# Performance work log

Hardware: AMD Instinct MI355X
Metric: run time of the kernel (lower is better)

## Reference

```python
import jax, jax.numpy as jnp
import numpy as np

D = 1024        # inputsize / d_model
G = 8           # groupnum (KV groups)
H = 16          # heads per group
DQ = 128        # qk head dim
DV = 128        # v head dim
FF = 1024       # ffoutsize
B, S = 1, 1024


def _rmsnorm(t, gamma, d_model):
    # torch F.normalize(x, dim=-1) * sqrt(d_model) * gamma
    n = jnp.sqrt(jnp.sum(t * t, axis=-1, keepdims=True))
    return t / jnp.maximum(n, 1e-12) * (d_model ** 0.5) * gamma


def setup_inputs() -> dict:
    key = jax.random.key(0)
    ks = jax.random.split(key, 8)
    std = 0.02
    x = jax.random.normal(ks[0], (B, S, D), dtype=jnp.float32)
    gamma_in = jnp.ones((D,), jnp.float32)
    Wq_w = jax.random.normal(ks[1], (H * G * DQ, D), jnp.float32) * std
    Wq_b = jnp.zeros((H * G * DQ,), jnp.float32)
    Wkv_w = jax.random.normal(ks[2], (G * (DQ + DV), D), jnp.float32) * std
    Wkv_b = jnp.zeros((G * (DQ + DV),), jnp.float32)
    gamma_z = jnp.ones((G * H * DV,), jnp.float32)
    W1 = jax.random.normal(ks[3], (FF * 2, G * H * DV), jnp.float32) * std
    b1 = jnp.zeros((FF * 2,), jnp.float32)
    W2 = jax.random.normal(ks[4], (FF, FF * 2), jnp.float32) * std
    b2 = jnp.zeros((FF,), jnp.float32)
    return {"x": x, "gamma_in": gamma_in, "Wq_w": Wq_w, "Wq_b": Wq_b,
            "Wkv_w": Wkv_w, "Wkv_b": Wkv_b, "gamma_z": gamma_z,
            "W1": W1, "b1": b1, "W2": W2, "b2": b2}


def reference(x, gamma_in, Wq_w, Wq_b, Wkv_w, Wkv_b, gamma_z, W1, b1, W2, b2):
    x = _rmsnorm(x, gamma_in, D)                      # (B,S,D)
    # self-attention path (m is None -> m = x)
    q = (x @ Wq_w.T + Wq_b).reshape(B, S, G, H, DQ)   # (B,S,G,H,dq)
    kv = x @ Wkv_w.T + Wkv_b                          # (B,S,G*(dq+dv))
    k, v = jnp.split(kv, 2, axis=-1)
    k = k.reshape(B, S, G, DQ)                        # (B,S,G,dq)
    v = v.reshape(B, S, G, DV)                        # (B,S,G,dv)
    scale = 1.0 / (DQ ** 0.5)
    scores = jnp.einsum('bsghd,bTgd->bghsT', q, k) * scale  # (B,G,H,S,S)
    attn = jax.nn.softmax(scores, axis=-1)
    z = jnp.einsum('bghsT,bTgd->bsghd', attn, v)      # (B,S,G,H,dv)
    z = z.reshape(B, S, G * H * DV)
    z = _rmsnorm(z, gamma_z, G * H * DV)
    h1 = jax.nn.silu(z @ W1.T + b1)                   # (B,S,2*FF)
    out = jax.nn.silu(h1 @ W2.T + b2)                 # (B,S,FF)
    return out
```

## Files before the change

### kernel.cpp

```cpp
#include <hip/hip_runtime.h>
#include <hip/hip_bf16.h>
#include <math.h>

typedef __attribute__((ext_vector_type(8))) short short8;
typedef __attribute__((ext_vector_type(4))) float floatx4;

__device__ __forceinline__ ushort f2bf(float f) {
  __hip_bfloat16 h = __float2bfloat16(f);
  return *reinterpret_cast<ushort*>(&h);
}
__device__ __forceinline__ float bf2f(ushort u) {
  union { unsigned int i; float f; } c; c.i = ((unsigned)u) << 16; return c.f;
}

__device__ __forceinline__ void lds_dma16(const void* g, void* l) {
  __builtin_amdgcn_global_load_lds((const __attribute__((address_space(1))) void*)g,
                                   (__attribute__((address_space(3))) void*)l, 16, 0, 0);
}

__global__ __launch_bounds__(256) void cvt_all(const float* __restrict__ p0, ushort* __restrict__ o0, int b0,
                                               const float* __restrict__ p1, ushort* __restrict__ o1, int b1,
                                               const float* __restrict__ p2, ushort* __restrict__ o2, int b2,
                                               const float* __restrict__ p3, ushort* __restrict__ o3) {
  int b = blockIdx.x;
  const float* in; ushort* out; int base;
  if (b < b0)            { in = p0; out = o0; base = 0; }
  else if (b < b0 + b1)  { in = p1; out = o1; base = b0; }
  else if (b < b0 + b1 + b2) { in = p2; out = o2; base = b0 + b1; }
  else                   { in = p3; out = o3; base = b0 + b1 + b2; }
  int i = (b - base) * 256 + threadIdx.x;
  float4 v = ((const float4*)in)[i];
  ushort4 o;
  o.x = f2bf(v.x); o.y = f2bf(v.y); o.z = f2bf(v.z); o.w = f2bf(v.w);
  ((ushort4*)out)[i] = o;
}

__global__ __launch_bounds__(256) void rmsnorm_f32(const float* __restrict__ x,
                                                   const float* __restrict__ gamma,
                                                   ushort* __restrict__ y, int D, float sqrtD) {
  const int row = blockIdx.x;
  const float* xr = x + (size_t)row * D;
  float ss = 0.f;
  for (int i = threadIdx.x * 4; i < D; i += 1024) {
    float4 v = *(const float4*)&xr[i];
    ss += v.x * v.x + v.y * v.y + v.z * v.z + v.w * v.w;
  }
#pragma unroll
  for (int off = 1; off < 64; off <<= 1) ss += __shfl_xor(ss, off);
  __shared__ float red[4];
  if ((threadIdx.x & 63) == 0) red[threadIdx.x >> 6] = ss;
  __syncthreads();
  ss = red[0] + red[1] + red[2] + red[3];
  const float sc = sqrtD / fmaxf(sqrtf(ss), 1e-12f);
  for (int i = threadIdx.x * 4; i < D; i += 1024) {
    float4 v = *(const float4*)&xr[i];
    ushort4 o;
    o.x = f2bf(v.x * sc * gamma[i]);
    o.y = f2bf(v.y * sc * gamma[i + 1]);
    o.z = f2bf(v.z * sc * gamma[i + 2]);
    o.w = f2bf(v.w * sc * gamma[i + 3]);
    *(ushort4*)&y[(size_t)row * D + i] = o;
  }
}

__global__ __launch_bounds__(256) void rmsnorm_bf16(const ushort* __restrict__ x,
                                                    const float* __restrict__ gamma,
                                                    ushort* __restrict__ y, int D, float sqrtD) {
  const int row = blockIdx.x;
  const ushort* xr = x + (size_t)row * D;
  short8 v[8];
  float ss = 0.f;
#pragma unroll
  for (int j = 0; j < 8; j++) {
    v[j] = *(const short8*)&xr[threadIdx.x * 8 + j * 2048];
#pragma unroll
    for (int e = 0; e < 8; e++) { float f = bf2f((ushort)v[j][e]); ss += f * f; }
  }
#pragma unroll
  for (int off = 1; off < 64; off <<= 1) ss += __shfl_xor(ss, off);
  __shared__ float red[4];
  if ((threadIdx.x & 63) == 0) red[threadIdx.x >> 6] = ss;
  __syncthreads();
  ss = red[0] + red[1] + red[2] + red[3];
  const float sc = sqrtD / fmaxf(sqrtf(ss), 1e-12f);
#pragma unroll
  for (int j = 0; j < 8; j++) {
    const int i = threadIdx.x * 8 + j * 2048;
    short8 ov;
#pragma unroll
    for (int e = 0; e < 8; e++) ov[e] = (short)f2bf(bf2f((ushort)v[j][e]) * sc * gamma[i + e]);
    *(short8*)&y[(size_t)row * D + i] = ov;
  }
}

template <int EPI, int ACT, int OUTBF16>
__global__ __launch_bounds__(256, 3) void gemm3(const ushort* __restrict__ A,
                                                const ushort* __restrict__ B,
                                                const float* __restrict__ bias,
                                                const float* __restrict__ bias2,
                                                void* __restrict__ C1,
                                                void* __restrict__ C2,
                                                int M, int N, int K, int Ksplit, float scale) {
  __shared__ ushort As[128 * 64];
  __shared__ ushort Bs[128 * 64];
  const int tid = threadIdx.x;
  const int wave = tid >> 6;
  const int lane = tid & 63;
  const int c16 = lane & 15;
  const int quad = lane >> 4;
  const int wm = wave >> 1;
  const int wn = wave & 1;
  const int P = gridDim.x * gridDim.y;
  const int lin = blockIdx.x + gridDim.x * blockIdx.y;
  const int lin2 = (lin & 7) * (P >> 3) + (lin >> 3);
  const int bx = lin2 & 7;
  const int by = lin2 >> 3;
  const size_t m0 = (size_t)bx * 128;
  const size_t n0 = (size_t)by * 128;
  const int kbeg = blockIdx.z * Ksplit;
  const int kend = kbeg + Ksplit;

  const int rsub = lane >> 3;
  const int csw = (lane & 7) ^ rsub;

  const floatx4 zero = {0.f, 0.f, 0.f, 0.f};
  floatx4 acc[4][4];
#pragma unroll
  for (int a = 0; a < 4; a++)
#pragma unroll
    for (int b = 0; b < 4; b++) acc[a][b] = zero;

  for (int k0 = kbeg; k0 < kend; k0 += 64) {
    __syncthreads();
#pragma unroll
    for (int i = 0; i < 4; i++) {
      const int j = wave * 4 + i;
      const int r = j * 8 + rsub;
      lds_dma16(&A[(m0 + r) * K + k0 + csw * 8], (void*)(As + j * 512));
      lds_dma16(&B[(n0 + r) * K + k0 + csw * 8], (void*)(Bs + j * 512));
    }
    __syncthreads();
#pragma unroll
    for (int kc = 0; kc < 2; kc++) {
      short8 af[4], bf4[4];
#pragma unroll
      for (int mt = 0; mt < 4; mt++) {
        const int row = wm * 64 + mt * 16 + c16;
        af[mt] = *(const short8*)&As[row * 64 + (((kc * 4 + quad) ^ (row & 7)) << 3)];
      }
#pragma unroll
      for (int nt = 0; nt < 4; nt++) {
        const int row = wn * 64 + nt * 16 + c16;
        bf4[nt] = *(const short8*)&Bs[row * 64 + (((kc * 4 + quad) ^ (row & 7)) << 3)];
      }
#pragma unroll
      for (int mt = 0; mt < 4; mt++)
#pragma unroll
        for (int nt = 0; nt < 4; nt++)
          acc[mt][nt] = __builtin_amdgcn_mfma_f32_16x16x32_bf16(af[mt], bf4[nt], acc[mt][nt], 0, 0, 0);
    }
  }

#pragma unroll
  for (int mt = 0; mt < 4; mt++) {
#pragma unroll
    for (int nt = 0; nt < 4; nt++) {
      const size_t col = n0 + wn * 64 + nt * 16 + c16;
      const size_t row0 = m0 + wm * 64 + mt * 16 + quad * 4;
      if (EPI == 0) {
        const float bv = bias[col];
#pragma unroll
        for (int r = 0; r < 4; r++) {
          float v = acc[mt][nt][r] + bv;
          if (ACT) v = v / (1.f + __expf(-v));
          if (OUTBF16) ((ushort*)C1)[(row0 + r) * N + col] = f2bf(v);
          else         ((float*)C1)[(row0 + r) * N + col] = v;
        }
      } else if (EPI == 1) {
        float* plane = (float*)C1 + (size_t)blockIdx.z * M * N;
#pragma unroll
        for (int r = 0; r < 4; r++)
          plane[(row0 + r) * N + col] = acc[mt][nt][r];
      } else {
        if (col < 16384) {
          const float bv = bias[col];
#pragma unroll
          for (int r = 0; r < 4; r++)
            ((ushort*)C1)[(row0 + r) * 16384 + col] = f2bf((acc[mt][nt][r] + bv) * scale);
        } else {
          const size_t ckv = col - 16384;
          const float bv = bias2[ckv];
#pragma unroll
          for (int r = 0; r < 4; r++)
            ((ushort*)C2)[(row0 + r) * 2048 + ckv] = f2bf(acc[mt][nt][r] + bv);
        }
      }
    }
  }
}

template <int NZ, int OUTBF16>
__global__ __launch_bounds__(256) void epi_sum_silu(const float* __restrict__ accb,
                                                    const float* __restrict__ bias,
                                                    void* __restrict__ outp, int N, int n4,
                                                    size_t plane4) {
  int i = blockIdx.x * 256 + threadIdx.x;
  if (i >= n4) return;
  float4 v = ((const float4*)accb)[i];
#pragma unroll
  for (int z = 1; z < NZ; z++) {
    float4 p = ((const float4*)accb)[i + z * plane4];
    v.x += p.x; v.y += p.y; v.z += p.z; v.w += p.w;
  }
  const float4 b = *(const float4*)&bias[(i * 4) % N];
  v.x += b.x; v.y += b.y; v.z += b.z; v.w += b.w;
  v.x = v.x / (1.f + __expf(-v.x));
  v.y = v.y / (1.f + __expf(-v.y));
  v.z = v.z / (1.f + __expf(-v.z));
  v.w = v.w / (1.f + __expf(-v.w));
  if (OUTBF16) {
    ushort4 o; o.x = f2bf(v.x); o.y = f2bf(v.y); o.z = f2bf(v.z); o.w = f2bf(v.w);
    ((ushort4*)outp)[i] = o;
  } else {
    ((float4*)outp)[i] = v;
  }
}

__global__ __launch_bounds__(256) void vtrans(const ushort* __restrict__ KV,
                                              ushort* __restrict__ VT) {
  __shared__ ushort Vl[64 * 138];
  const int tid = threadIdx.x;
  const int t0 = blockIdx.x * 64;
  const int g = blockIdx.y;
#pragma unroll
  for (int i = 0; i < 16; i++) {
    int idx = tid + i * 256;
    int r = idx >> 6, dc = idx & 63;
    *(uint*)&Vl[r * 138 + dc * 2] =
        *(const uint*)&KV[(size_t)(t0 + r) * 2048 + 1024 + g * 128 + dc * 2];
  }
  __syncthreads();
#pragma unroll
  for (int i = 0; i < 4; i++) {
    int idx = tid + i * 256;
    int dv = idx >> 3, tch = idx & 7;
    short8 o;
#pragma unroll
    for (int j = 0; j < 8; j++) o[j] = (short)Vl[(tch * 8 + j) * 138 + dv];
    *(short8*)&VT[(size_t)g * 131072 + (size_t)dv * 1024 + t0 + tch * 8] = o;
  }
}

__global__ __launch_bounds__(512, 4) void attn9(const ushort* __restrict__ Q,
                                                const ushort* __restrict__ KV,
                                                const ushort* __restrict__ VT,
                                                ushort* __restrict__ Z) {
  __shared__ ushort Kl[2][64 * 128];
  __shared__ ushort Vt[128 * 64];
  __shared__ ushort Pl[128 * 64];
  float* Ls = (float*)Pl;
  const int tid = threadIdx.x;
  const int w = tid >> 6;
  const int lane = tid & 63;
  const int c16 = lane & 15;
  const int quad = lane >> 4;
  const int b = (blockIdx.x & 7) * 128 + (blockIdx.x >> 3);
  const int hh = b >> 3;
  const int qb = b & 7;
  const int g = hh >> 4;
  const int prow0 = (w & 3) * 32;
  const int dv0 = (w >> 2) * 64;

  const ushort* Kg = KV + (size_t)g * 128;
  const ushort* Vg = VT + (size_t)g * 131072;

  short8 aq[4];
#pragma unroll
  for (int kc = 0; kc < 4; kc++)
    aq[kc] = *(const short8*)&Q[(size_t)(qb * 128 + w * 16 + c16) * 16384 +
                                hh * 128 + kc * 32 + quad * 8];

  const floatx4 zero = {0.f, 0.f, 0.f, 0.f};
  floatx4 o[2][4];
  float lacc[4];
#pragma unroll
  for (int mt = 0; mt < 2; mt++)
#pragma unroll
    for (int nt = 0; nt < 4; nt++) o[mt][nt] = zero;
#pragma unroll
  for (int r = 0; r < 4; r++) lacc[r] = 0.f;

  const int kr16 = lane >> 4;
  const int kc16 = lane & 15;
  const int vr8 = lane >> 3;
  const int vc8 = lane & 7;

  auto stageK = [&](int buf, int t0) {
#pragma unroll
    for (int i = 0; i < 2; i++) {
      int krow = w * 8 + i * 4 + kr16;
      int kcs = kc16 ^ (krow & 7);
      lds_dma16(&Kg[(size_t)(t0 + krow) * 2048 + kcs * 8],
                (void*)(&Kl[buf][w * 1024 + i * 512]));
    }
  };
  auto stageV = [&](int t0) {
#pragma unroll
    for (int i = 0; i < 2; i++) {
      int vrow = w * 16 + i * 8 + vr8;
      int vcs = vc8 ^ (vrow & 7);
      lds_dma16(&Vg[(size_t)vrow * 1024 + t0 + vcs * 8],
                (void*)(&Vt[w * 1024 + i * 512]));
    }
  };

  stageK(0, 0);

  for (int t = 0; t < 16; t++) {
    const int p = t & 1;
    __syncthreads();
    if (t < 15) stageK(p ^ 1, (t + 1) * 64);
    stageV(t * 64);

#pragma unroll
    for (int st = 0; st < 4; st++) {
      floatx4 s0 = zero;
      const int krow = st * 16 + c16;
      __builtin_amdgcn_s_setprio(1);
#pragma unroll
      for (int kc = 0; kc < 4; kc++) {
        short8 bk = *(const short8*)&Kl[p][krow * 128 + (((kc * 4 + quad) ^ (c16 & 7)) << 3)];
        s0 = __builtin_amdgcn_mfma_f32_16x16x32_bf16(aq[kc], bk, s0, 0, 0, 0);
      }
      __builtin_amdgcn_s_setprio(0);
#pragma unroll
      for (int r = 0; r < 4; r++) {
        float p0 = __expf(s0[r]);
        lacc[r] += p0;
        const int rlo = w * 16 + quad * 4 + r;
        const int sw = ((((st * 2) + (c16 >> 3)) ^ (rlo & 7)) << 3) | (c16 & 7);
        Pl[rlo * 64 + sw] = f2bf(p0);
      }
    }
    __syncthreads();

#pragma unroll
    for (int tc = 0; tc < 2; tc++) {
      short8 ap[2];
#pragma unroll
      for (int mt = 0; mt < 2; mt++) {
        const int row = prow0 + mt * 16 + c16;
        ap[mt] = *(const short8*)&Pl[row * 64 + (((tc * 4 + quad) ^ (c16 & 7)) << 3)];
      }
      __builtin_amdgcn_s_setprio(1);
#pragma unroll
      for (int nt = 0; nt < 4; nt++) {
        const int dv = dv0 + nt * 16 + c16;
        short8 bv = *(const short8*)&Vt[dv * 64 + (((tc * 4 + quad) ^ (c16 & 7)) << 3)];
#pragma unroll
        for (int mt = 0; mt < 2; mt++)
          o[mt][nt] = __builtin_amdgcn_mfma_f32_16x16x32_bf16(ap[mt], bv, o[mt][nt], 0, 0, 0);
      }
      __builtin_amdgcn_s_setprio(0);
    }
  }

  __syncthreads();
#pragma unroll
  for (int r = 0; r < 4; r++) {
    float l = lacc[r];
    l += __shfl_xor(l, 1);
    l += __shfl_xor(l, 2);
    l += __shfl_xor(l, 4);
    l += __shfl_xor(l, 8);
    if (c16 == 0) Ls[w * 16 + quad * 4 + r] = l;
  }
  __syncthreads();

#pragma unroll
  for (int mt = 0; mt < 2; mt++) {
#pragma unroll
    for (int r = 0; r < 4; r++) {
      const float inv = 1.f / Ls[prow0 + mt * 16 + quad * 4 + r];
      const size_t row = (size_t)qb * 128 + prow0 + mt * 16 + quad * 4 + r;
#pragma unroll
      for (int nt = 0; nt < 4; nt++)
        Z[row * 16384 + hh * 128 + dv0 + nt * 16 + c16] = f2bf(o[mt][nt][r] * inv);
    }
  }
}

extern "C" void kernel_launch(void* const* d_in, const int* in_sizes, int n_in,
                              void* d_out, int out_size, void* d_ws, size_t ws_size,
                              hipStream_t stream) {
  (void)in_sizes; (void)n_in; (void)out_size;
  const float* x        = (const float*)d_in[0];
  const float* gamma_in = (const float*)d_in[1];
  const float* Wq_w     = (const float*)d_in[2];
  const float* Wq_b     = (const float*)d_in[3];
  const float* Wkv_w    = (const float*)d_in[4];
  const float* Wkv_b    = (const float*)d_in[5];
  const float* gamma_z  = (const float*)d_in[6];
  const float* W1       = (const float*)d_in[7];
  const float* b1       = (const float*)d_in[8];
  const float* W2       = (const float*)d_in[9];
  const float* b2       = (const float*)d_in[10];
  float* out = (float*)d_out;

  const size_t MB = 1024 * 1024;
  char* ws = (char*)d_ws;
  const bool big = ws_size >= 174 * MB;

  ushort *xn, *Wqb, *Wkvb, *W1b, *W2b, *Qb, *KVb, *Zb, *VTb, *ZN, *H1;
  float *h1f, *outf;
  size_t off = 0;
  auto alloc = [&](size_t bytes) {
    void* p = ws + off;
    off += (bytes + 255) & ~(size_t)255;
    return p;
  };
  if (big) {
    xn   = (ushort*)alloc(2 * MB);
    W1b  = (ushort*)alloc(64 * MB);
    W2b  = (ushort*)alloc(4 * MB);
    Qb   = (ushort*)alloc(32 * MB);
    KVb  = (ushort*)alloc(4 * MB);
    Wqb  = (ushort*)alloc(32 * MB);
    Wkvb = (ushort*)alloc(4 * MB);
    Zb   = (ushort*)alloc(32 * MB);
    VTb  = Wkvb;
    ZN   = Qb;
    h1f  = (float*)Wqb;
    H1   = KVb;
    outf = (float*)Qb;
  } else {
    xn   = (ushort*)alloc(2 * MB);
    Wqb  = (ushort*)alloc(32 * MB);
    Wkvb = (ushort*)alloc(4 * MB);
    W1b  = (ushort*)alloc(64 * MB);
    W2b  = (ushort*)alloc(4 * MB);
    Qb   = (ushort*)alloc(32 * MB);
    KVb  = (ushort*)alloc(4 * MB);
    Zb   = Wqb;
    VTb  = Wkvb;
    ZN   = Qb;
    h1f  = (float*)Wqb;
    H1   = Wkvb;
    outf = (float*)Qb;
  }

  cvt_all<<<16384 + 2048 + 32768 + 2048, 256, 0, stream>>>(
      Wq_w, Wqb, 16384, Wkv_w, Wkvb, 2048, W1, W1b, 32768, W2, W2b);

  rmsnorm_f32<<<1024, 256, 0, stream>>>(x, gamma_in, xn, 1024, 32.0f);

  { dim3 g(8, 144, 1);
    gemm3<2, 0, 1><<<g, 256, 0, stream>>>(xn, Wqb, Wq_b, Wkv_b, Qb, KVb,
                                          1024, 18432, 1024, 1024, 0.08838834764831845f); }

  { dim3 g(16, 8); vtrans<<<g, 256, 0, stream>>>(KVb, VTb); }

  attn9<<<1024, 512, 0, stream>>>(Qb, KVb, VTb, Zb);

  rmsnorm_bf16<<<1024, 256, 0, stream>>>(Zb, gamma_z, ZN, 16384, 128.0f);

  if (big) {
    dim3 g(8, 16, 8);
    gemm3<1, 0, 0><<<g, 256, 0, stream>>>(ZN, W1b, b1, nullptr, h1f, nullptr,
                                          1024, 2048, 16384, 2048, 0.f);
    epi_sum_silu<8, 1><<<2048, 256, 0, stream>>>(h1f, b1, H1, 2048, 1024 * 2048 / 4,
                                                 (size_t)1024 * 2048 / 4);
  } else {
    dim3 g(8, 16, 4);
    gemm3<1, 0, 0><<<g, 256, 0, stream>>>(ZN, W1b, b1, nullptr, h1f, nullptr,
                                          1024, 2048, 16384, 4096, 0.f);
    epi_sum_silu<4, 1><<<2048, 256, 0, stream>>>(h1f, b1, H1, 2048, 1024 * 2048 / 4,
                                                 (size_t)1024 * 2048 / 4);
  }

  { dim3 g(8, 8, 8);
    gemm3<1, 0, 0><<<g, 256, 0, stream>>>(H1, W2b, b2, nullptr, outf, nullptr,
                                          1024, 1024, 2048, 256, 0.f); }
  epi_sum_silu<8, 0><<<1024, 256, 0, stream>>>(outf, b2, out, 1024, 1024 * 1024 / 4,
                                               (size_t)1024 * 1024 / 4);
}
```

Baseline: 581.7 us.

## Add 256x256 split-K GEMM with interleaved LDS staging for W1 projection

Adds a new 512-thread GEMM kernel that computes 256x256 tiles and double-buffers them in LDS through async global-to-LDS loads. Loads for the next K tile are interleaved with four compute phases, and the MFMA phases are raised in priority so memory and math overlap. The kernel replaces the generic gemm3 for the large z@W1 split-K product. The W2 GEMM also drops from split-K 8 to 4, which halves the partial-plane traffic in its epilogue. The trade-offs are a larger LDS footprint and fewer blocks, which may lower occupancy.

```diff
diff --git a/kernel.cpp b/kernel.cpp
--- a/kernel.cpp
+++ b/kernel.cpp
@@ -195,6 +195,128 @@
             ((ushort*)C2)[(row0 + r) * 2048 + ckv] = f2bf(acc[mt][nt][r] + bv);
         }
       }
+    }
+  }
+}
+
+#define GP8_COMPUTE_PAIR(Q)                                                          \
+  {                                                                                  \
+    __builtin_amdgcn_s_setprio(1);                                                   \
+    _Pragma("unroll")                                                                \
+    for (int m2 = 0; m2 < 2; m2++) {                                                 \
+      const int mt = (Q) * 2 + m2;                                                   \
+      const int row = wm * 128 + mt * 16 + c16;                                      \
+      _Pragma("unroll")                                                              \
+      for (int kc = 0; kc < 2; kc++) {                                               \
+        short8 af = *(const short8*)&Al[buf][row * 64 + (((kc * 4 + quad) ^ (row & 7)) << 3)]; \
+        _Pragma("unroll")                                                            \
+        for (int nt = 0; nt < 4; nt++)                                               \
+          acc[(Q) * 2 + m2][nt] =                                                    \
+              __builtin_amdgcn_mfma_f32_16x16x32_bf16(af, bf[nt][kc], acc[(Q) * 2 + m2][nt], 0, 0, 0); \
+      }                                                                              \
+    }                                                                                \
+    __builtin_amdgcn_s_setprio(0);                                                   \
+  }
+
+__global__ __launch_bounds__(512, 2) void gemm8p(const ushort* __restrict__ A,
+                                                 const ushort* __restrict__ B,
+                                                 float* __restrict__ planes,
+                                                 int M, int N, int K, int Ksplit) {
+  __shared__ ushort Al[2][256 * 64];
+  __shared__ ushort Bl[2][256 * 64];
+  const int tid = threadIdx.x;
+  const int w = tid >> 6;
+  const int lane = tid & 63;
+  const int c16 = lane & 15;
+  const int quad = lane >> 4;
+  const int wm = w >> 2;
+  const int wn = w & 3;
+  const int rsub = lane >> 3;
+  const int csw = (lane & 7) ^ rsub;
+
+  const int P = gridDim.x * gridDim.y;
+  const int lin = blockIdx.x + gridDim.x * blockIdx.y;
+  const int lin2 = (lin & 7) * (P >> 3) + (lin >> 3);
+  const size_t m0 = (size_t)(lin2 & 3) * 256;
+  const size_t n0 = (size_t)(lin2 >> 2) * 256;
+  const int kbeg = blockIdx.z * Ksplit;
+  const int nkt = Ksplit >> 6;
+
+  const floatx4 zero = {0.f, 0.f, 0.f, 0.f};
+  floatx4 acc[8][4];
+#pragma unroll
+  for (int a = 0; a < 8; a++)
+#pragma unroll
+    for (int b = 0; b < 4; b++) acc[a][b] = zero;
+
+  auto stageA = [&](int bu, int h, int k0) {
+#pragma unroll
+    for (int i = 0; i < 2; i++) {
+      const int j = w * 2 + i;
+      const int r = h * 128 + j * 8 + rsub;
+      lds_dma16(&A[(m0 + r) * K + k0 + csw * 8], (void*)(&Al[bu][h * 8192 + j * 512]));
+    }
+  };
+  auto stageB = [&](int bu, int h, int k0) {
+#pragma unroll
+    for (int i = 0; i < 2; i++) {
+      const int j = w * 2 + i;
+      const int r = h * 128 + j * 8 + rsub;
+      lds_dma16(&B[(n0 + r) * K + k0 + csw * 8], (void*)(&Bl[bu][h * 8192 + j * 512]));
+    }
+  };
+
+  stageA(0, 0, kbeg); stageB(0, 0, kbeg); stageA(0, 1, kbeg); stageB(0, 1, kbeg);
+
+  short8 bf[4][2];
+
+  for (int kt = 0; kt < nkt; kt++) {
+    const int buf = kt & 1;
+    const int kn = kbeg + (kt + 1) * 64;
+    const bool more = (kt + 1 < nkt);
+
+    if (more) {
+      stageA(buf ^ 1, 0, kn);
+      asm volatile("s_waitcnt vmcnt(2) lgkmcnt(0)\n\ts_barrier" ::: "memory");
+    } else {
+      asm volatile("s_waitcnt vmcnt(0) lgkmcnt(0)\n\ts_barrier" ::: "memory");
+    }
+#pragma unroll
+    for (int nt = 0; nt < 4; nt++)
+#pragma unroll
+      for (int kc = 0; kc < 2; kc++) {
+        const int row = wn * 64 + nt * 16 + c16;
+        bf[nt][kc] = *(const short8*)&Bl[buf][row * 64 + (((kc * 4 + quad) ^ (row & 7)) << 3)];
+      }
+    GP8_COMPUTE_PAIR(0)
+    asm volatile("s_barrier" ::: "memory");
+
+    if (more) stageB(buf ^ 1, 0, kn);
+    asm volatile("s_barrier" ::: "memory");
+    GP8_COMPUTE_PAIR(1)
+    asm volatile("s_barrier" ::: "memory");
+
+    if (more) stageA(buf ^ 1, 1, kn);
+    asm volatile("s_barrier" ::: "memory");
+    GP8_COMPUTE_PAIR(2)
+    asm volatile("s_barrier" ::: "memory");
+
+    if (more) stageB(buf ^ 1, 1, kn);
+    asm volatile("s_barrier" ::: "memory");
+    GP8_COMPUTE_PAIR(3)
+    asm volatile("s_barrier" ::: "memory");
+  }
+
+  float* plane = planes + (size_t)blockIdx.z * M * N;
+#pragma unroll
+  for (int mt = 0; mt < 8; mt++) {
+#pragma unroll
+    for (int nt = 0; nt < 4; nt++) {
+      const size_t col = n0 + wn * 64 + nt * 16 + c16;
+      const size_t row0 = m0 + wm * 128 + mt * 16 + quad * 4;
+#pragma unroll
+      for (int r = 0; r < 4; r++)
+        plane[(row0 + r) * N + col] = acc[mt][nt][r];
     }
   }
 }
@@ -465,9 +587,8 @@
   rmsnorm_bf16<<<1024, 256, 0, stream>>>(Zb, gamma_z, ZN, 16384, 128.0f);
 
   if (big) {
-    dim3 g(8, 16, 8);
-    gemm3<1, 0, 0><<<g, 256, 0, stream>>>(ZN, W1b, b1, nullptr, h1f, nullptr,
-                                          1024, 2048, 16384, 2048, 0.f);
+    dim3 g(4, 8, 8);
+    gemm8p<<<g, 512, 0, stream>>>(ZN, W1b, h1f, 1024, 2048, 16384, 2048);
     epi_sum_silu<8, 1><<<2048, 256, 0, stream>>>(h1f, b1, H1, 2048, 1024 * 2048 / 4,
                                                  (size_t)1024 * 2048 / 4);
   } else {
@@ -478,9 +599,9 @@
                                                  (size_t)1024 * 2048 / 4);
   }
 
-  { dim3 g(8, 8, 8);
+  { dim3 g(8, 8, 4);
     gemm3<1, 0, 0><<<g, 256, 0, stream>>>(H1, W2b, b2, nullptr, outf, nullptr,
-                                          1024, 1024, 2048, 256, 0.f); }
-  epi_sum_silu<8, 0><<<1024, 256, 0, stream>>>(outf, b2, out, 1024, 1024 * 1024 / 4,
+                                          1024, 1024, 2048, 512, 0.f); }
+  epi_sum_silu<4, 0><<<1024, 256, 0, stream>>>(outf, b2, out, 1024, 1024 * 1024 / 4,
                                                (size_t)1024 * 1024 / 4);
 }
```

After: 599.8 us. +3.1%, slower.
